# Kernel optimization log

Hardware: AMD Instinct MI355X
Metric: run time of the kernel (lower is better)

Reference implementation:

```python
import jax, jax.numpy as jnp
import numpy as np

B, S, E, H = 2, 2048, 1024, 16
HD = E // H


def setup_inputs() -> dict:
    key = jax.random.key(0)
    ks = jax.random.split(key, 5)
    scale = 1.0 / np.sqrt(E)
    return {
        "query": jax.random.normal(ks[0], (B, S, E), jnp.float32),
        "key": jax.random.normal(ks[1], (B, S, E), jnp.float32),
        "value": jax.random.normal(ks[2], (B, S, E), jnp.float32),
        "qkv_w": jax.random.normal(ks[3], (3 * E, E), jnp.float32) * scale,
        "qkv_b": jnp.zeros((3 * E,), jnp.float32),
        "out_w": jax.random.normal(ks[4], (E, E), jnp.float32) * scale,
        "out_b": jnp.zeros((E,), jnp.float32),
    }


def reference(query, key, value, qkv_w, qkv_b, out_w, out_b):
    # Fused QKV projection from query (module ignores key/value contents)
    qkv = query @ qkv_w.T + qkv_b                      # [B,S,3E]
    qkv = qkv.reshape(B, S, 3, H, HD)
    q = qkv[:, :, 0].transpose(0, 2, 1, 3)             # [B,H,S,HD]
    k = qkv[:, :, 1].transpose(0, 2, 1, 3)
    v = qkv[:, :, 2].transpose(0, 2, 1, 3)
    scaling = 1.0 / np.sqrt(HD)
    scores = jnp.einsum("bhqd,bhkd->bhqk", q, k) * scaling  # [B,H,S,S]
    probs = jax.nn.softmax(scores, axis=-1)
    ctx = jnp.einsum("bhqk,bhkd->bhqd", probs, v)      # [B,H,S,HD]
    ctx = ctx.transpose(0, 2, 1, 3).reshape(B, S, E)
    return ctx @ out_w.T + out_b
```

## Files before the change

### kernel.cpp

```cpp
#include <hip/hip_runtime.h>
#include <hip/hip_bf16.h>
#include <math.h>

#define BB 2
#define SS 2048
#define EE 1024
#define HH 16
#define HD 64

typedef __bf16 bf16;
typedef __bf16 bf16x8 __attribute__((ext_vector_type(8)));
typedef float floatx4 __attribute__((ext_vector_type(4)));
typedef float floatx16 __attribute__((ext_vector_type(16)));

#define MFMA(a, b, c) __builtin_amdgcn_mfma_f32_16x16x32_bf16(a, b, c, 0, 0, 0)
#define MFMA32(a, b, c) __builtin_amdgcn_mfma_f32_32x32x16_bf16(a, b, c, 0, 0, 0)

__device__ inline void async16(const bf16* g, bf16* l) {
    __builtin_amdgcn_global_load_lds(
        (const __attribute__((address_space(1))) void*)g,
        (__attribute__((address_space(3))) void*)l, 16, 0, 0);
}

__device__ inline unsigned cvt_pk_bf16(float a, float b) {
    unsigned r;
    asm("v_cvt_pk_bf16_f32 %0, %1, %2" : "=v"(r) : "v"(a), "v"(b));
    return r;
}

__device__ inline float fast_exp2(float x) {
    float r;
    asm("v_exp_f32 %0, %1" : "=v"(r) : "v"(x));
    return r;
}

__global__ __launch_bounds__(256) void cvt3(
    const float* __restrict__ a, const float* __restrict__ b,
    const float* __restrict__ c,
    bf16* __restrict__ oa, bf16* __restrict__ ob, bf16* __restrict__ oc) {
    const long NA = (long)4096 * 1024, NB = (long)3072 * 1024, NC = (long)1024 * 1024;
    const long total = (NA + NB + NC) >> 2;
    long i = (long)blockIdx.x * blockDim.x + threadIdx.x;
    const long stride = (long)gridDim.x * blockDim.x;
    for (; i < total; i += stride) {
        const long e = i << 2;
        const float* src;
        bf16* dst;
        if (e < NA)           { src = a + e;            dst = oa + e; }
        else if (e < NA + NB) { src = b + (e - NA);     dst = ob + (e - NA); }
        else                  { src = c + (e - NA - NB); dst = oc + (e - NA - NB); }
        float4 v = *(const float4*)src;
        union { bf16 h[4]; uint2 u; } t;
        t.h[0] = (bf16)v.x; t.h[1] = (bf16)v.y; t.h[2] = (bf16)v.z; t.h[3] = (bf16)v.w;
        *(uint2*)dst = t.u;
    }
}

__global__ __launch_bounds__(256) void qkv_gemm(
    const bf16* __restrict__ A, const bf16* __restrict__ W,
    const float* __restrict__ bias,
    bf16* __restrict__ Qw, bf16* __restrict__ Kw, bf16* __restrict__ Vtw) {
    __shared__ __align__(16) bf16 As[2][128 * 64];
    __shared__ __align__(16) bf16 Bs[2][128 * 64];
    const int tid  = threadIdx.x;
    const int wave = tid >> 6, lane = tid & 63;
    const int quad = lane >> 4, l16 = lane & 15;
    const int wr = wave >> 1, wc = wave & 1;
    const int m0 = blockIdx.y * 128, n0 = blockIdx.x * 128;
    const int lr = lane >> 3;
    const int lcs = ((lane & 7) ^ (lr & 7)) * 8;
    const int rsw = (l16 & 7) << 3;

    const bf16* Ag = A + (long)(m0 + wave * 32 + lr) * 1024 + lcs;
    const bf16* Bg = W + (long)(n0 + wave * 32 + lr) * 1024 + lcs;
    const int lbase = (wave * 32) * 64 + lane * 8;

    floatx4 acc[4][4] = {};

#pragma unroll
    for (int j = 0; j < 4; ++j) {
        async16(Ag + (long)j * 8 * 1024, &As[0][lbase + j * 8 * 64]);
        async16(Bg + (long)j * 8 * 1024, &Bs[0][lbase + j * 8 * 64]);
    }

    for (int ks = 0; ks < 16; ++ks) {
        __syncthreads();
        const int cur = ks & 1;
        if (ks < 15) {
            const int nxt = cur ^ 1, k0 = (ks + 1) * 64;
#pragma unroll
            for (int j = 0; j < 4; ++j) {
                async16(Ag + (long)j * 8 * 1024 + k0, &As[nxt][lbase + j * 8 * 64]);
                async16(Bg + (long)j * 8 * 1024 + k0, &Bs[nxt][lbase + j * 8 * 64]);
            }
        }
#pragma unroll
        for (int c = 0; c < 2; ++c) {
            bf16x8 af[4], bfr[4];
#pragma unroll
            for (int mi = 0; mi < 4; ++mi)
                af[mi] = *(const bf16x8*)&As[cur][(wr * 64 + mi * 16 + l16) * 64 + ((c * 32 + quad * 8) ^ rsw)];
#pragma unroll
            for (int ni = 0; ni < 4; ++ni)
                bfr[ni] = *(const bf16x8*)&Bs[cur][(wc * 64 + ni * 16 + l16) * 64 + ((c * 32 + quad * 8) ^ rsw)];
#pragma unroll
            for (int mi = 0; mi < 4; ++mi)
#pragma unroll
                for (int ni = 0; ni < 4; ++ni)
                    acc[mi][ni] = MFMA(af[mi], bfr[ni], acc[mi][ni]);
        }
    }

#pragma unroll
    for (int mi = 0; mi < 4; ++mi)
#pragma unroll
        for (int ni = 0; ni < 4; ++ni) {
            const int n = n0 + wc * 64 + ni * 16 + l16;
            const float bn = bias[n];
            const int sel = n >> 10;
            const int e = n & 1023, h = e >> 6, d = e & 63;
            if (sel == 2) {
                const int m_base = m0 + wr * 64 + mi * 16 + quad * 4;
                const int b = m_base >> 11, s0 = m_base & 2047;
                union { bf16 h4[4]; uint2 u; } t;
#pragma unroll
                for (int r = 0; r < 4; ++r)
                    t.h4[r] = (bf16)(acc[mi][ni][r] + bn);
                *(uint2*)&Vtw[((long)(b * HH + h) * HD + d) * SS + s0] = t.u;
            } else {
#pragma unroll
                for (int r = 0; r < 4; ++r) {
                    const int m = m0 + wr * 64 + mi * 16 + quad * 4 + r;
                    const int b = m >> 11, s = m & 2047;
                    const float v = acc[mi][ni][r] + bn;
                    if (sel == 0)
                        Qw[((long)(b * HH + h) * SS + s) * HD + d] = (bf16)(v * 0.18033688f);
                    else
                        Kw[((long)(b * HH + h) * SS + s) * HD + d] = (bf16)v;
                }
            }
        }
}

__global__ __launch_bounds__(512) void attn(
    const bf16* __restrict__ Qw, const bf16* __restrict__ Kw,
    const bf16* __restrict__ Vtw, bf16* __restrict__ ctxw) {
    extern __shared__ __align__(16) bf16 smem[];

    const int tid = threadIdx.x;
    const int wave = tid >> 6, lane = tid & 63;
    const int grp = wave >> 2, w4 = wave & 3;
    const int l5 = lane & 31, hi = lane >> 5;

    const int d_  = blockIdx.y * gridDim.x + blockIdx.x;
    const int j_  = d_ >> 3;
    const int bh  = (d_ & 7) * 4 + (j_ >> 4);
    const int qb  = j_ & 15;

    const bf16* Qh = Qw  + (long)bh * SS * HD;
    const bf16* Kh = Kw  + (long)bh * SS * HD;
    const bf16* Vh = Vtw + (long)bh * HD * SS;

    const int qbase = qb * 128 + w4 * 32;
    bf16x8 qf[4];
#pragma unroll
    for (int d0 = 0; d0 < 4; ++d0)
        qf[d0] = *(const bf16x8*)&Qh[(long)(qbase + l5) * HD + d0 * 16 + hi * 8];

    floatx16 ctx0 = {}, ctx1 = {};
    float lsum = 0.f;

    const int wrow = w4 * 8 + (lane >> 3);
    const int sch  = ((lane & 7) ^ ((lane >> 3) & 7)) * 8;
    const int kvo  = grp * 1024;
    const bf16* Kg0 = Kh + (long)(kvo + wrow) * HD + sch;
    const bf16* Kg1 = Kh + (long)(kvo + 32 + wrow) * HD + sch;
    const bf16* Vg0 = Vh + (long)wrow * SS + kvo + sch;
    const bf16* Vg1 = Vh + (long)(32 + wrow) * SS + kvo + sch;
    const int ldst = w4 * 512 + lane * 8;
    const int rswz = (l5 & 7) << 3;

    bf16* Kt0 = smem + (grp * 2 + 0) * 4096;
    bf16* Kt1 = smem + (grp * 2 + 1) * 4096;
    bf16* Vt0 = smem + 16384 + (grp * 2 + 0) * 4096;
    bf16* Vt1 = smem + 16384 + (grp * 2 + 1) * 4096;

    async16(Kg0, Kt0 + ldst);
    async16(Kg1, Kt0 + ldst + 2048);
    async16(Vg0, Vt0 + ldst);
    async16(Vg1, Vt0 + ldst + 2048);

    for (int kt = 0; kt < 16; ++kt) {
        __syncthreads();

        if (kt < 15) {
            bf16* Kn = (kt & 1) ? Kt0 : Kt1;
            bf16* Vn = (kt & 1) ? Vt0 : Vt1;
            const long ko = (long)(kt + 1) * 64;
            async16(Kg0 + ko * HD, Kn + ldst);
            async16(Kg1 + ko * HD, Kn + ldst + 2048);
            async16(Vg0 + ko,      Vn + ldst);
            async16(Vg1 + ko,      Vn + ldst + 2048);
        }
        const bf16* Kc = (kt & 1) ? Kt1 : Kt0;
        const bf16* Vc = (kt & 1) ? Vt1 : Vt0;

        floatx16 sf[2];
#pragma unroll
        for (int kb = 0; kb < 2; ++kb) {
            floatx16 s = {};
            __builtin_amdgcn_s_setprio(1);
#pragma unroll
            for (int d0 = 0; d0 < 4; ++d0) {
                const bf16x8 af = *(const bf16x8*)
                    &Kc[(kb * 32 + l5) * 64 + ((d0 * 16 + hi * 8) ^ rswz)];
                s = MFMA32(af, qf[d0], s);
            }
            __builtin_amdgcn_s_setprio(0);
            sf[kb] = s;
        }

#pragma unroll
        for (int kb = 0; kb < 2; ++kb) {
#pragma unroll
            for (int r = 0; r < 16; ++r) {
                const float p = fast_exp2(sf[kb][r]);
                sf[kb][r] = p;
                lsum += p;
            }
            unsigned w[8];
#pragma unroll
            for (int i = 0; i < 8; ++i)
                w[i] = cvt_pk_bf16(sf[kb][2 * i], sf[kb][2 * i + 1]);
            asm("v_permlane32_swap_b32 %0, %1" : "+v"(w[0]), "+v"(w[2]));
            asm("v_permlane32_swap_b32 %0, %1" : "+v"(w[1]), "+v"(w[3]));
            asm("v_permlane32_swap_b32 %0, %1" : "+v"(w[4]), "+v"(w[6]));
            asm("v_permlane32_swap_b32 %0, %1" : "+v"(w[5]), "+v"(w[7]));
            union { unsigned u[4]; bf16x8 v; } pa0 = {{w[0], w[1], w[2], w[3]}},
                                               pa1 = {{w[4], w[5], w[6], w[7]}};
#pragma unroll
            for (int kc = 0; kc < 2; ++kc) {
                const bf16x8 pa = kc ? pa1.v : pa0.v;
                const int kcol = kb * 32 + kc * 16 + hi * 8;
                const bf16x8 vf0 = *(const bf16x8*)&Vc[l5 * 64 + (kcol ^ rswz)];
                const bf16x8 vf1 = *(const bf16x8*)&Vc[(32 + l5) * 64 + (kcol ^ rswz)];
                __builtin_amdgcn_s_setprio(1);
                ctx0 = MFMA32(pa, vf0, ctx0);
                ctx1 = MFMA32(pa, vf1, ctx1);
                __builtin_amdgcn_s_setprio(0);
            }
        }
    }

    __syncthreads();
    float* cb = (float*)smem;
    float* lb = (float*)(smem + 16384);
    if (grp == 1) {
#pragma unroll
        for (int r = 0; r < 16; ++r) {
            cb[(w4 * 32 + r) * 64 + lane]      = ctx0[r];
            cb[(w4 * 32 + 16 + r) * 64 + lane] = ctx1[r];
        }
        lb[w4 * 64 + lane] = lsum;
    }
    __syncthreads();
    if (grp == 0) {
        lsum += lb[w4 * 64 + lane];
#pragma unroll
        for (int r = 0; r < 16; ++r) {
            ctx0[r] += cb[(w4 * 32 + r) * 64 + lane];
            ctx1[r] += cb[(w4 * 32 + 16 + r) * 64 + lane];
        }
        const float rs  = lsum + __shfl_xor(lsum, 32, 64);
        const float inv = 1.0f / rs;

        const int b = bh >> 4, h = bh & 15;
#pragma unroll
        for (int r = 0; r < 16; ++r) {
            const int qrow = (r & 3) + 8 * (r >> 2) + 4 * hi;
            const float iq = __shfl(inv, qrow, 64);
            const long base = ((long)b * SS + qbase + qrow) * EE + h * HD;
            ctxw[base + l5]      = (bf16)(ctx0[r] * iq);
            ctxw[base + 32 + l5] = (bf16)(ctx1[r] * iq);
        }
    }
}

__global__ __launch_bounds__(256) void out_gemm(
    const bf16* __restrict__ A, const bf16* __restrict__ W,
    const float* __restrict__ bias, float* __restrict__ out) {
    __shared__ __align__(16) bf16 As[2][64 * 64];
    __shared__ __align__(16) bf16 Bs[2][128 * 64];
    const int tid  = threadIdx.x;
    const int wave = tid >> 6, lane = tid & 63;
    const int quad = lane >> 4, l16 = lane & 15;
    const int wr = wave & 1, wc = wave >> 1;
    const int m0 = blockIdx.y * 64, n0 = blockIdx.x * 128;
    const int lr = lane >> 3;
    const int lcs = ((lane & 7) ^ (lr & 7)) * 8;
    const int rsw = (l16 & 7) << 3;

    const bf16* Ag = A + (long)(m0 + wave * 16 + lr) * 1024 + lcs;
    const bf16* Bg = W + (long)(n0 + wave * 32 + lr) * 1024 + lcs;
    const int labase = (wave * 16) * 64 + lane * 8;
    const int lbbase = (wave * 32) * 64 + lane * 8;

    floatx4 acc[2][4] = {};

#pragma unroll
    for (int j = 0; j < 2; ++j)
        async16(Ag + (long)j * 8 * 1024, &As[0][labase + j * 8 * 64]);
#pragma unroll
    for (int j = 0; j < 4; ++j)
        async16(Bg + (long)j * 8 * 1024, &Bs[0][lbbase + j * 8 * 64]);

    for (int ks = 0; ks < 16; ++ks) {
        __syncthreads();
        const int cur = ks & 1;
        if (ks < 15) {
            const int nxt = cur ^ 1, k0 = (ks + 1) * 64;
#pragma unroll
            for (int j = 0; j < 2; ++j)
                async16(Ag + (long)j * 8 * 1024 + k0, &As[nxt][labase + j * 8 * 64]);
#pragma unroll
            for (int j = 0; j < 4; ++j)
                async16(Bg + (long)j * 8 * 1024 + k0, &Bs[nxt][lbbase + j * 8 * 64]);
        }
#pragma unroll
        for (int c = 0; c < 2; ++c) {
            bf16x8 af[2], bfr[4];
#pragma unroll
            for (int mi = 0; mi < 2; ++mi)
                af[mi] = *(const bf16x8*)&As[cur][(wr * 32 + mi * 16 + l16) * 64 + ((c * 32 + quad * 8) ^ rsw)];
#pragma unroll
            for (int ni = 0; ni < 4; ++ni)
                bfr[ni] = *(const bf16x8*)&Bs[cur][(wc * 64 + ni * 16 + l16) * 64 + ((c * 32 + quad * 8) ^ rsw)];
#pragma unroll
            for (int mi = 0; mi < 2; ++mi)
#pragma unroll
                for (int ni = 0; ni < 4; ++ni)
                    acc[mi][ni] = MFMA(af[mi], bfr[ni], acc[mi][ni]);
        }
    }

#pragma unroll
    for (int mi = 0; mi < 2; ++mi)
#pragma unroll
        for (int ni = 0; ni < 4; ++ni) {
            const int n = n0 + wc * 64 + ni * 16 + l16;
            const float bn = bias[n];
#pragma unroll
            for (int r = 0; r < 4; ++r) {
                const int m = m0 + wr * 32 + mi * 16 + quad * 4 + r;
                out[(long)m * 1024 + n] = acc[mi][ni][r] + bn;
            }
        }
}

extern "C" void kernel_launch(void* const* d_in, const int* in_sizes, int n_in,
                              void* d_out, int out_size, void* d_ws, size_t ws_size,
                              hipStream_t stream) {
    const float* query = (const float*)d_in[0];
    const float* qkv_w = (const float*)d_in[3];
    const float* qkv_b = (const float*)d_in[4];
    const float* out_w = (const float*)d_in[5];
    const float* out_b = (const float*)d_in[6];

    const long NTOK = (long)BB * SS;
    bf16* qb   = (bf16*)d_ws;
    bf16* wqb  = qb  + NTOK * EE;
    bf16* owb  = wqb + (long)3 * EE * EE;
    bf16* Qw   = owb + (long)EE * EE;
    bf16* Kw   = Qw  + NTOK * EE;
    bf16* Vtw  = Kw  + NTOK * EE;
    bf16* ctxw = qb;
    float* out = (float*)d_out;

    cvt3<<<2048, 256, 0, stream>>>(query, qkv_w, out_w, qb, wqb, owb);
    qkv_gemm<<<dim3(24, 32), 256, 0, stream>>>(qb, wqb, qkv_b, Qw, Kw, Vtw);
    attn<<<dim3(16, 32), 512, 65536, stream>>>(Qw, Kw, Vtw, ctxw);
    out_gemm<<<dim3(8, 64), 256, 0, stream>>>(ctxw, owb, out_b, out);
}
```

Measured before the change: 208.3 us.

## Make QKV GEMM persistent with 512-thread blocks and split-role loading

The QKV projection GEMM moves from a 24x32 grid of 256-thread blocks to a persistent grid of 512 blocks of 512 threads, each looping over 128x128 output tiles. Half the waves stage A tiles and half stage W tiles, and each of the eight waves now computes a 64x32 sub-tile instead of 64x64. This is meant to raise occupancy and latency hiding by spreading the MFMA work over more waves. The cost is an uneven tail, since 768 tiles over 512 blocks leaves some blocks doing two tiles and others one, plus an extra barrier per tile.

```diff
diff --git a/kernel.cpp b/kernel.cpp
--- a/kernel.cpp
+++ b/kernel.cpp
@@ -7,6 +7,7 @@
 #define EE 1024
 #define HH 16
 #define HD 64
+#define NBLK 512
 
 typedef __bf16 bf16;
 typedef __bf16 bf16x8 __attribute__((ext_vector_type(8)));
@@ -56,90 +57,93 @@
     }
 }
 
-__global__ __launch_bounds__(256) void qkv_gemm(
+__global__ __launch_bounds__(512, 4) void qkv_gemm(
     const bf16* __restrict__ A, const bf16* __restrict__ W,
     const float* __restrict__ bias,
     bf16* __restrict__ Qw, bf16* __restrict__ Kw, bf16* __restrict__ Vtw) {
-    __shared__ __align__(16) bf16 As[2][128 * 64];
-    __shared__ __align__(16) bf16 Bs[2][128 * 64];
+    __shared__ __align__(16) bf16 smem[32768];
+    const int bid  = blockIdx.x;
     const int tid  = threadIdx.x;
     const int wave = tid >> 6, lane = tid & 63;
     const int quad = lane >> 4, l16 = lane & 15;
-    const int wr = wave >> 1, wc = wave & 1;
-    const int m0 = blockIdx.y * 128, n0 = blockIdx.x * 128;
+    const int wr = wave >> 2, wc = wave & 3;
     const int lr = lane >> 3;
     const int lcs = ((lane & 7) ^ (lr & 7)) * 8;
     const int rsw = (l16 & 7) << 3;
-
-    const bf16* Ag = A + (long)(m0 + wave * 32 + lr) * 1024 + lcs;
-    const bf16* Bg = W + (long)(n0 + wave * 32 + lr) * 1024 + lcs;
-    const int lbase = (wave * 32) * 64 + lane * 8;
-
-    floatx4 acc[4][4] = {};
-
-#pragma unroll
-    for (int j = 0; j < 4; ++j) {
-        async16(Ag + (long)j * 8 * 1024, &As[0][lbase + j * 8 * 64]);
-        async16(Bg + (long)j * 8 * 1024, &Bs[0][lbase + j * 8 * 64]);
-    }
-
-    for (int ks = 0; ks < 16; ++ks) {
+    bf16* As0 = smem;         bf16* As1 = smem + 8192;
+    bf16* Bs0 = smem + 16384; bf16* Bs1 = smem + 24576;
+    const bool stA = wave < 4;
+    const int sw = wave & 3;
+    bf16* L0g = (stA ? As0 : Bs0) + sw * 2048 + lane * 8;
+    bf16* L1g = (stA ? As1 : Bs1) + sw * 2048 + lane * 8;
+
+    for (int tile = bid; tile < 768; tile += NBLK) {
+        const int m0 = (tile / 24) * 128, n0 = (tile % 24) * 128;
+        const bf16* G = stA
+            ? (A + (long)(m0 + sw * 32 + lr) * 1024 + lcs)
+            : (W + (long)(n0 + sw * 32 + lr) * 1024 + lcs);
+        floatx4 acc[4][2] = {};
+#pragma unroll
+        for (int j = 0; j < 4; ++j)
+            async16(G + (long)j * 8 * 1024, L0g + j * 512);
+        for (int ks = 0; ks < 16; ++ks) {
+            __syncthreads();
+            if (ks < 15) {
+                bf16* Ln = (ks & 1) ? L0g : L1g;
+                const int k0 = (ks + 1) * 64;
+#pragma unroll
+                for (int j = 0; j < 4; ++j)
+                    async16(G + (long)j * 8 * 1024 + k0, Ln + j * 512);
+            }
+            const bf16* Ac = (ks & 1) ? As1 : As0;
+            const bf16* Bc = (ks & 1) ? Bs1 : Bs0;
+#pragma unroll
+            for (int c = 0; c < 2; ++c) {
+                bf16x8 af[4], bfr[2];
+#pragma unroll
+                for (int mi = 0; mi < 4; ++mi)
+                    af[mi] = *(const bf16x8*)&Ac[(wr * 64 + mi * 16 + l16) * 64 + ((c * 32 + quad * 8) ^ rsw)];
+#pragma unroll
+                for (int ni = 0; ni < 2; ++ni)
+                    bfr[ni] = *(const bf16x8*)&Bc[(wc * 32 + ni * 16 + l16) * 64 + ((c * 32 + quad * 8) ^ rsw)];
+#pragma unroll
+                for (int mi = 0; mi < 4; ++mi)
+#pragma unroll
+                    for (int ni = 0; ni < 2; ++ni)
+                        acc[mi][ni] = MFMA(af[mi], bfr[ni], acc[mi][ni]);
+            }
+        }
+#pragma unroll
+        for (int mi = 0; mi < 4; ++mi)
+#pragma unroll
+            for (int ni = 0; ni < 2; ++ni) {
+                const int n = n0 + wc * 32 + ni * 16 + l16;
+                const float bn = bias[n];
+                const int sel = n >> 10;
+                const int e = n & 1023, h = e >> 6, d = e & 63;
+                if (sel == 2) {
+                    const int m_base = m0 + wr * 64 + mi * 16 + quad * 4;
+                    const int b = m_base >> 11, s0 = m_base & 2047;
+                    union { bf16 h4[4]; uint2 u; } t;
+#pragma unroll
+                    for (int r = 0; r < 4; ++r)
+                        t.h4[r] = (bf16)(acc[mi][ni][r] + bn);
+                    *(uint2*)&Vtw[((long)(b * HH + h) * HD + d) * SS + s0] = t.u;
+                } else {
+#pragma unroll
+                    for (int r = 0; r < 4; ++r) {
+                        const int m = m0 + wr * 64 + mi * 16 + quad * 4 + r;
+                        const int b = m >> 11, s = m & 2047;
+                        const float v = acc[mi][ni][r] + bn;
+                        if (sel == 0)
+                            Qw[((long)(b * HH + h) * SS + s) * HD + d] = (bf16)(v * 0.18033688f);
+                        else
+                            Kw[((long)(b * HH + h) * SS + s) * HD + d] = (bf16)v;
+                    }
+                }
+            }
         __syncthreads();
-        const int cur = ks & 1;
-        if (ks < 15) {
-            const int nxt = cur ^ 1, k0 = (ks + 1) * 64;
-#pragma unroll
-            for (int j = 0; j < 4; ++j) {
-                async16(Ag + (long)j * 8 * 1024 + k0, &As[nxt][lbase + j * 8 * 64]);
-                async16(Bg + (long)j * 8 * 1024 + k0, &Bs[nxt][lbase + j * 8 * 64]);
-            }
-        }
-#pragma unroll
-        for (int c = 0; c < 2; ++c) {
-            bf16x8 af[4], bfr[4];
-#pragma unroll
-            for (int mi = 0; mi < 4; ++mi)
-                af[mi] = *(const bf16x8*)&As[cur][(wr * 64 + mi * 16 + l16) * 64 + ((c * 32 + quad * 8) ^ rsw)];
-#pragma unroll
-            for (int ni = 0; ni < 4; ++ni)
-                bfr[ni] = *(const bf16x8*)&Bs[cur][(wc * 64 + ni * 16 + l16) * 64 + ((c * 32 + quad * 8) ^ rsw)];
-#pragma unroll
-            for (int mi = 0; mi < 4; ++mi)
-#pragma unroll
-                for (int ni = 0; ni < 4; ++ni)
-                    acc[mi][ni] = MFMA(af[mi], bfr[ni], acc[mi][ni]);
-        }
-    }
-
-#pragma unroll
-    for (int mi = 0; mi < 4; ++mi)
-#pragma unroll
-        for (int ni = 0; ni < 4; ++ni) {
-            const int n = n0 + wc * 64 + ni * 16 + l16;
-            const float bn = bias[n];
-            const int sel = n >> 10;
-            const int e = n & 1023, h = e >> 6, d = e & 63;
-            if (sel == 2) {
-                const int m_base = m0 + wr * 64 + mi * 16 + quad * 4;
-                const int b = m_base >> 11, s0 = m_base & 2047;
-                union { bf16 h4[4]; uint2 u; } t;
-#pragma unroll
-                for (int r = 0; r < 4; ++r)
-                    t.h4[r] = (bf16)(acc[mi][ni][r] + bn);
-                *(uint2*)&Vtw[((long)(b * HH + h) * HD + d) * SS + s0] = t.u;
-            } else {
-#pragma unroll
-                for (int r = 0; r < 4; ++r) {
-                    const int m = m0 + wr * 64 + mi * 16 + quad * 4 + r;
-                    const int b = m >> 11, s = m & 2047;
-                    const float v = acc[mi][ni][r] + bn;
-                    if (sel == 0)
-                        Qw[((long)(b * HH + h) * SS + s) * HD + d] = (bf16)(v * 0.18033688f);
-                    else
-                        Kw[((long)(b * HH + h) * SS + s) * HD + d] = (bf16)v;
-                }
-            }
-        }
+    }
 }
 
 __global__ __launch_bounds__(512) void attn(
@@ -192,7 +196,6 @@
 
     for (int kt = 0; kt < 16; ++kt) {
         __syncthreads();
-
         if (kt < 15) {
             bf16* Kn = (kt & 1) ? Kt0 : Kt1;
             bf16* Vn = (kt & 1) ? Vt0 : Vt1;
@@ -377,7 +380,7 @@
     float* out = (float*)d_out;
 
     cvt3<<<2048, 256, 0, stream>>>(query, qkv_w, out_w, qb, wqb, owb);
-    qkv_gemm<<<dim3(24, 32), 256, 0, stream>>>(qb, wqb, qkv_b, Qw, Kw, Vtw);
+    qkv_gemm<<<dim3(NBLK), dim3(512), 0, stream>>>(qb, wqb, qkv_b, Qw, Kw, Vtw);
     attn<<<dim3(16, 32), 512, 65536, stream>>>(Qw, Kw, Vtw, ctxw);
     out_gemm<<<dim3(8, 64), 256, 0, stream>>>(ctxw, owb, out_b, out);
 }
```

Result: faster. 198.9 us (-4.5%).
